# Kernel tuning notes

Measured on AMD Instinct MI355X. Metric: run time of the kernel, lower is better.

## Reference

```python
import jax, jax.numpy as jnp
import numpy as np

TOKENS = 131072
DIM = 512
NUM_EXPERTS = 4
TOPK = 2
ROUTE_SCALE = 1.0


def setup_inputs() -> dict:
    key = jax.random.key(0)
    k1, k2, k3 = jax.random.split(key, 3)
    x = jax.random.normal(k1, (TOKENS, DIM), dtype=jnp.float32)
    weight = jax.random.normal(k2, (NUM_EXPERTS, DIM), dtype=jnp.float32) * 0.02
    bias = jax.random.normal(k3, (NUM_EXPERTS,), dtype=jnp.float32) * 0.01
    return {"x": x, "weight": weight, "bias": bias}


def reference(x, weight, bias):
    # scores = x @ W^T -> [T, E]
    logits = jnp.einsum('td,ed->te', x, weight)
    scores = jax.nn.softmax(logits.astype(jnp.float32), axis=-1)  # fp32 softmax
    biased = scores + bias  # bias only affects expert selection
    _, indices = jax.lax.top_k(biased, TOPK)  # [T, topk] int32
    weights = jnp.take_along_axis(scores, indices, axis=1) * ROUTE_SCALE
    return weights.astype(x.dtype), indices
```

## Files before the change

kernel.cpp:

```cpp
#include <hip/hip_runtime.h>
#include <math.h>


constexpr int TOKENS = 131072;
constexpr int DIM = 512;

__global__ __launch_bounds__(256) void gate_kernel(
    const float* __restrict__ x,
    const float* __restrict__ w,
    const float* __restrict__ bias,
    float* __restrict__ out_w,
    float* __restrict__ out_i)
{
    const int lane   = threadIdx.x & 63;
    const int wavesPerBlock = blockDim.x >> 6;
    const int wave   = blockIdx.x * wavesPerBlock + (threadIdx.x >> 6);
    const int nwaves = gridDim.x * wavesPerBlock;

    float4 w0a, w0b, w1a, w1b, w2a, w2b, w3a, w3b;
    {
        const float4* wp0 = reinterpret_cast<const float4*>(w + 0 * DIM + lane * 8);
        const float4* wp1 = reinterpret_cast<const float4*>(w + 1 * DIM + lane * 8);
        const float4* wp2 = reinterpret_cast<const float4*>(w + 2 * DIM + lane * 8);
        const float4* wp3 = reinterpret_cast<const float4*>(w + 3 * DIM + lane * 8);
        w0a = wp0[0]; w0b = wp0[1];
        w1a = wp1[0]; w1b = wp1[1];
        w2a = wp2[0]; w2b = wp2[1];
        w3a = wp3[0]; w3b = wp3[1];
    }
    const float b0 = bias[0], b1 = bias[1], b2 = bias[2], b3 = bias[3];

    for (int t = wave; t < TOKENS; t += nwaves) {
        const float4* xp = reinterpret_cast<const float4*>(x + (size_t)t * DIM + lane * 8);
        const float4 xa = xp[0];
        const float4 xb = xp[1];

        float a0 = xa.x * w0a.x + xa.y * w0a.y + xa.z * w0a.z + xa.w * w0a.w
                 + xb.x * w0b.x + xb.y * w0b.y + xb.z * w0b.z + xb.w * w0b.w;
        float a1 = xa.x * w1a.x + xa.y * w1a.y + xa.z * w1a.z + xa.w * w1a.w
                 + xb.x * w1b.x + xb.y * w1b.y + xb.z * w1b.z + xb.w * w1b.w;
        float a2 = xa.x * w2a.x + xa.y * w2a.y + xa.z * w2a.z + xa.w * w2a.w
                 + xb.x * w2b.x + xb.y * w2b.y + xb.z * w2b.z + xb.w * w2b.w;
        float a3 = xa.x * w3a.x + xa.y * w3a.y + xa.z * w3a.z + xa.w * w3a.w
                 + xb.x * w3b.x + xb.y * w3b.y + xb.z * w3b.z + xb.w * w3b.w;

        #pragma unroll
        for (int off = 1; off < 64; off <<= 1) {
            a0 += __shfl_xor(a0, off, 64);
            a1 += __shfl_xor(a1, off, 64);
            a2 += __shfl_xor(a2, off, 64);
            a3 += __shfl_xor(a3, off, 64);
        }

        const float m  = fmaxf(fmaxf(a0, a1), fmaxf(a2, a3));
        const float e0 = __expf(a0 - m);
        const float e1 = __expf(a1 - m);
        const float e2 = __expf(a2 - m);
        const float e3 = __expf(a3 - m);
        const float inv = 1.0f / (e0 + e1 + e2 + e3);
        const float s0 = e0 * inv, s1 = e1 * inv, s2 = e2 * inv, s3 = e3 * inv;

        const float p0 = s0 + b0, p1 = s1 + b1, p2 = s2 + b2, p3 = s3 + b3;

        int   i0 = 0; float bv0 = p0, sv0 = s0;
        if (p1 > bv0) { bv0 = p1; sv0 = s1; i0 = 1; }
        if (p2 > bv0) { bv0 = p2; sv0 = s2; i0 = 2; }
        if (p3 > bv0) { bv0 = p3; sv0 = s3; i0 = 3; }
        int   i1 = -1; float bv1 = -INFINITY, sv1 = 0.0f;
        if (i0 != 0 && p0 > bv1) { bv1 = p0; sv1 = s0; i1 = 0; }
        if (i0 != 1 && p1 > bv1) { bv1 = p1; sv1 = s1; i1 = 1; }
        if (i0 != 2 && p2 > bv1) { bv1 = p2; sv1 = s2; i1 = 2; }
        if (i0 != 3 && p3 > bv1) { bv1 = p3; sv1 = s3; i1 = 3; }

        if (lane == 0) {
            float2 wv = make_float2(sv0, sv1);
            float2 iv = make_float2((float)i0, (float)i1);
            *reinterpret_cast<float2*>(out_w + 2 * (size_t)t) = wv;
            *reinterpret_cast<float2*>(out_i + 2 * (size_t)t) = iv;
        }
    }
}

extern "C" void kernel_launch(void* const* d_in, const int* in_sizes, int n_in,
                              void* d_out, int out_size, void* d_ws, size_t ws_size,
                              hipStream_t stream) {
    const float* x    = (const float*)d_in[0];
    const float* w    = (const float*)d_in[1];
    const float* bias = (const float*)d_in[2];

    float* out_w = (float*)d_out;
    float* out_i = (float*)d_out + (size_t)TOKENS * 2;

    const int block  = 256;
    const int blocks = 2048;
    gate_kernel<<<blocks, block, 0, stream>>>(x, w, bias, out_w, out_i);
}
```

Measured before the change: 49.62 us.

## Process token pairs per wave with contiguous chunks and nontemporal loads

Replaces the grid-stride loop with fixed contiguous 16-token chunks per wave. Each iteration handles two tokens at once with interleaved shuffle reductions, and the combined results are written as float4 stores. x is now read with nontemporal loads using a lo/hi column split, so each lane loads contiguous 16-byte pieces across the wave. The grid is resized to cover the token count exactly and an occupancy hint is added to launch_bounds. The aim is more memory-level parallelism and less cache pollution on a bandwidth-bound streaming read, at the cost of more registers.

```diff
diff --git a/kernel.cpp b/kernel.cpp
--- a/kernel.cpp
+++ b/kernel.cpp
@@ -4,79 +4,120 @@
 
 constexpr int TOKENS = 131072;
 constexpr int DIM = 512;
+constexpr int CHUNK = 16;
 
-__global__ __launch_bounds__(256) void gate_kernel(
+typedef float fvec4 __attribute__((ext_vector_type(4)));
+
+__global__ __launch_bounds__(256, 4) void gate_kernel(
     const float* __restrict__ x,
     const float* __restrict__ w,
     const float* __restrict__ bias,
     float* __restrict__ out_w,
     float* __restrict__ out_i)
 {
-    const int lane   = threadIdx.x & 63;
-    const int wavesPerBlock = blockDim.x >> 6;
-    const int wave   = blockIdx.x * wavesPerBlock + (threadIdx.x >> 6);
-    const int nwaves = gridDim.x * wavesPerBlock;
+    const int lane = threadIdx.x & 63;
+    const int wave = blockIdx.x * (blockDim.x >> 6) + (threadIdx.x >> 6);
+    const int t0   = wave * CHUNK;
 
-    float4 w0a, w0b, w1a, w1b, w2a, w2b, w3a, w3b;
-    {
-        const float4* wp0 = reinterpret_cast<const float4*>(w + 0 * DIM + lane * 8);
-        const float4* wp1 = reinterpret_cast<const float4*>(w + 1 * DIM + lane * 8);
-        const float4* wp2 = reinterpret_cast<const float4*>(w + 2 * DIM + lane * 8);
-        const float4* wp3 = reinterpret_cast<const float4*>(w + 3 * DIM + lane * 8);
-        w0a = wp0[0]; w0b = wp0[1];
-        w1a = wp1[0]; w1b = wp1[1];
-        w2a = wp2[0]; w2b = wp2[1];
-        w3a = wp3[0]; w3b = wp3[1];
-    }
+    const int cLo = 4 * lane;
+    const int cHi = 256 + 4 * lane;
+
+    const fvec4 w0a = *reinterpret_cast<const fvec4*>(w + 0 * DIM + cLo);
+    const fvec4 w0b = *reinterpret_cast<const fvec4*>(w + 0 * DIM + cHi);
+    const fvec4 w1a = *reinterpret_cast<const fvec4*>(w + 1 * DIM + cLo);
+    const fvec4 w1b = *reinterpret_cast<const fvec4*>(w + 1 * DIM + cHi);
+    const fvec4 w2a = *reinterpret_cast<const fvec4*>(w + 2 * DIM + cLo);
+    const fvec4 w2b = *reinterpret_cast<const fvec4*>(w + 2 * DIM + cHi);
+    const fvec4 w3a = *reinterpret_cast<const fvec4*>(w + 3 * DIM + cLo);
+    const fvec4 w3b = *reinterpret_cast<const fvec4*>(w + 3 * DIM + cHi);
     const float b0 = bias[0], b1 = bias[1], b2 = bias[2], b3 = bias[3];
 
-    for (int t = wave; t < TOKENS; t += nwaves) {
-        const float4* xp = reinterpret_cast<const float4*>(x + (size_t)t * DIM + lane * 8);
-        const float4 xa = xp[0];
-        const float4 xb = xp[1];
+    #pragma unroll
+    for (int j = 0; j < CHUNK; j += 2) {
+        const int tA = t0 + j;
+        const int tB = tA + 1;
+        const float* rowA = x + (size_t)tA * DIM;
+        const float* rowB = x + (size_t)tB * DIM;
 
-        float a0 = xa.x * w0a.x + xa.y * w0a.y + xa.z * w0a.z + xa.w * w0a.w
-                 + xb.x * w0b.x + xb.y * w0b.y + xb.z * w0b.z + xb.w * w0b.w;
-        float a1 = xa.x * w1a.x + xa.y * w1a.y + xa.z * w1a.z + xa.w * w1a.w
-                 + xb.x * w1b.x + xb.y * w1b.y + xb.z * w1b.z + xb.w * w1b.w;
-        float a2 = xa.x * w2a.x + xa.y * w2a.y + xa.z * w2a.z + xa.w * w2a.w
-                 + xb.x * w2b.x + xb.y * w2b.y + xb.z * w2b.z + xb.w * w2b.w;
-        float a3 = xa.x * w3a.x + xa.y * w3a.y + xa.z * w3a.z + xa.w * w3a.w
-                 + xb.x * w3b.x + xb.y * w3b.y + xb.z * w3b.z + xb.w * w3b.w;
+        const fvec4 xa0 = __builtin_nontemporal_load(reinterpret_cast<const fvec4*>(rowA + cLo));
+        const fvec4 xa1 = __builtin_nontemporal_load(reinterpret_cast<const fvec4*>(rowA + cHi));
+        const fvec4 xb0 = __builtin_nontemporal_load(reinterpret_cast<const fvec4*>(rowB + cLo));
+        const fvec4 xb1 = __builtin_nontemporal_load(reinterpret_cast<const fvec4*>(rowB + cHi));
+
+        float A0 = xa0.x*w0a.x + xa0.y*w0a.y + xa0.z*w0a.z + xa0.w*w0a.w
+                 + xa1.x*w0b.x + xa1.y*w0b.y + xa1.z*w0b.z + xa1.w*w0b.w;
+        float A1 = xa0.x*w1a.x + xa0.y*w1a.y + xa0.z*w1a.z + xa0.w*w1a.w
+                 + xa1.x*w1b.x + xa1.y*w1b.y + xa1.z*w1b.z + xa1.w*w1b.w;
+        float A2 = xa0.x*w2a.x + xa0.y*w2a.y + xa0.z*w2a.z + xa0.w*w2a.w
+                 + xa1.x*w2b.x + xa1.y*w2b.y + xa1.z*w2b.z + xa1.w*w2b.w;
+        float A3 = xa0.x*w3a.x + xa0.y*w3a.y + xa0.z*w3a.z + xa0.w*w3a.w
+                 + xa1.x*w3b.x + xa1.y*w3b.y + xa1.z*w3b.z + xa1.w*w3b.w;
+
+        float B0 = xb0.x*w0a.x + xb0.y*w0a.y + xb0.z*w0a.z + xb0.w*w0a.w
+                 + xb1.x*w0b.x + xb1.y*w0b.y + xb1.z*w0b.z + xb1.w*w0b.w;
+        float B1 = xb0.x*w1a.x + xb0.y*w1a.y + xb0.z*w1a.z + xb0.w*w1a.w
+                 + xb1.x*w1b.x + xb1.y*w1b.y + xb1.z*w1b.z + xb1.w*w1b.w;
+        float B2 = xb0.x*w2a.x + xb0.y*w2a.y + xb0.z*w2a.z + xb0.w*w2a.w
+                 + xb1.x*w2b.x + xb1.y*w2b.y + xb1.z*w2b.z + xb1.w*w2b.w;
+        float B3 = xb0.x*w3a.x + xb0.y*w3a.y + xb0.z*w3a.z + xb0.w*w3a.w
+                 + xb1.x*w3b.x + xb1.y*w3b.y + xb1.z*w3b.z + xb1.w*w3b.w;
 
         #pragma unroll
         for (int off = 1; off < 64; off <<= 1) {
-            a0 += __shfl_xor(a0, off, 64);
-            a1 += __shfl_xor(a1, off, 64);
-            a2 += __shfl_xor(a2, off, 64);
-            a3 += __shfl_xor(a3, off, 64);
+            A0 += __shfl_xor(A0, off, 64);
+            B0 += __shfl_xor(B0, off, 64);
+            A1 += __shfl_xor(A1, off, 64);
+            B1 += __shfl_xor(B1, off, 64);
+            A2 += __shfl_xor(A2, off, 64);
+            B2 += __shfl_xor(B2, off, 64);
+            A3 += __shfl_xor(A3, off, 64);
+            B3 += __shfl_xor(B3, off, 64);
         }
 
-        const float m  = fmaxf(fmaxf(a0, a1), fmaxf(a2, a3));
-        const float e0 = __expf(a0 - m);
-        const float e1 = __expf(a1 - m);
-        const float e2 = __expf(a2 - m);
-        const float e3 = __expf(a3 - m);
-        const float inv = 1.0f / (e0 + e1 + e2 + e3);
-        const float s0 = e0 * inv, s1 = e1 * inv, s2 = e2 * inv, s3 = e3 * inv;
+        float sA0, sA1, sA2, sA3;
+        {
+            const float m  = fmaxf(fmaxf(A0, A1), fmaxf(A2, A3));
+            const float e0 = __expf(A0 - m), e1 = __expf(A1 - m);
+            const float e2 = __expf(A2 - m), e3 = __expf(A3 - m);
+            const float inv = 1.0f / (e0 + e1 + e2 + e3);
+            sA0 = e0 * inv; sA1 = e1 * inv; sA2 = e2 * inv; sA3 = e3 * inv;
+        }
+        float sB0, sB1, sB2, sB3;
+        {
+            const float m  = fmaxf(fmaxf(B0, B1), fmaxf(B2, B3));
+            const float e0 = __expf(B0 - m), e1 = __expf(B1 - m);
+            const float e2 = __expf(B2 - m), e3 = __expf(B3 - m);
+            const float inv = 1.0f / (e0 + e1 + e2 + e3);
+            sB0 = e0 * inv; sB1 = e1 * inv; sB2 = e2 * inv; sB3 = e3 * inv;
+        }
 
-        const float p0 = s0 + b0, p1 = s1 + b1, p2 = s2 + b2, p3 = s3 + b3;
+        const float pA0 = sA0 + b0, pA1 = sA1 + b1, pA2 = sA2 + b2, pA3 = sA3 + b3;
+        int   iA0 = 0; float bvA = pA0, svA0 = sA0;
+        if (pA1 > bvA) { bvA = pA1; svA0 = sA1; iA0 = 1; }
+        if (pA2 > bvA) { bvA = pA2; svA0 = sA2; iA0 = 2; }
+        if (pA3 > bvA) { bvA = pA3; svA0 = sA3; iA0 = 3; }
+        int   iA1 = -1; float bvA1 = -INFINITY, svA1 = 0.0f;
+        if (iA0 != 0 && pA0 > bvA1) { bvA1 = pA0; svA1 = sA0; iA1 = 0; }
+        if (iA0 != 1 && pA1 > bvA1) { bvA1 = pA1; svA1 = sA1; iA1 = 1; }
+        if (iA0 != 2 && pA2 > bvA1) { bvA1 = pA2; svA1 = sA2; iA1 = 2; }
+        if (iA0 != 3 && pA3 > bvA1) { bvA1 = pA3; svA1 = sA3; iA1 = 3; }
 
-        int   i0 = 0; float bv0 = p0, sv0 = s0;
-        if (p1 > bv0) { bv0 = p1; sv0 = s1; i0 = 1; }
-        if (p2 > bv0) { bv0 = p2; sv0 = s2; i0 = 2; }
-        if (p3 > bv0) { bv0 = p3; sv0 = s3; i0 = 3; }
-        int   i1 = -1; float bv1 = -INFINITY, sv1 = 0.0f;
-        if (i0 != 0 && p0 > bv1) { bv1 = p0; sv1 = s0; i1 = 0; }
-        if (i0 != 1 && p1 > bv1) { bv1 = p1; sv1 = s1; i1 = 1; }
-        if (i0 != 2 && p2 > bv1) { bv1 = p2; sv1 = s2; i1 = 2; }
-        if (i0 != 3 && p3 > bv1) { bv1 = p3; sv1 = s3; i1 = 3; }
+        const float pB0 = sB0 + b0, pB1 = sB1 + b1, pB2 = sB2 + b2, pB3 = sB3 + b3;
+        int   iB0 = 0; float bvB = pB0, svB0 = sB0;
+        if (pB1 > bvB) { bvB = pB1; svB0 = sB1; iB0 = 1; }
+        if (pB2 > bvB) { bvB = pB2; svB0 = sB2; iB0 = 2; }
+        if (pB3 > bvB) { bvB = pB3; svB0 = sB3; iB0 = 3; }
+        int   iB1 = -1; float bvB1 = -INFINITY, svB1 = 0.0f;
+        if (iB0 != 0 && pB0 > bvB1) { bvB1 = pB0; svB1 = sB0; iB1 = 0; }
+        if (iB0 != 1 && pB1 > bvB1) { bvB1 = pB1; svB1 = sB1; iB1 = 1; }
+        if (iB0 != 2 && pB2 > bvB1) { bvB1 = pB2; svB1 = sB2; iB1 = 2; }
+        if (iB0 != 3 && pB3 > bvB1) { bvB1 = pB3; svB1 = sB3; iB1 = 3; }
 
         if (lane == 0) {
-            float2 wv = make_float2(sv0, sv1);
-            float2 iv = make_float2((float)i0, (float)i1);
-            *reinterpret_cast<float2*>(out_w + 2 * (size_t)t) = wv;
-            *reinterpret_cast<float2*>(out_i + 2 * (size_t)t) = iv;
+            fvec4 wv; wv.x = svA0; wv.y = svA1; wv.z = svB0; wv.w = svB1;
+            fvec4 iv; iv.x = (float)iA0; iv.y = (float)iA1; iv.z = (float)iB0; iv.w = (float)iB1;
+            *reinterpret_cast<fvec4*>(out_w + 2 * (size_t)tA) = wv;
+            *reinterpret_cast<fvec4*>(out_i + 2 * (size_t)tA) = iv;
         }
     }
 }
@@ -92,6 +133,6 @@
     float* out_i = (float*)d_out + (size_t)TOKENS * 2;
 
     const int block  = 256;
-    const int blocks = 2048;
+    const int blocks = TOKENS / (CHUNK * 4);
     gate_kernel<<<blocks, block, 0, stream>>>(x, w, bias, out_w, out_i);
 }
```

Result: slower. 56.80 us (+14.5%).
